# Performance work log

Hardware: AMD Instinct MI355X
Metric: run time of the kernel (lower is better)

The kernel has to match this reference:

```python
import jax, jax.numpy as jnp
import numpy as np

DIM = 128
HEADS = 4
POS_DIM = (DIM // 4) // 4  # DynamicPosBias: pos_dim = (dim//4)//4 = 8


def _layernorm(x, g, b, eps=1e-5):
    m = x.mean(-1, keepdims=True)
    v = x.var(-1, keepdims=True)
    return (x - m) / jnp.sqrt(v + eps) * g + b


def setup_inputs() -> dict:
    key = jax.random.key(0)
    ks = jax.random.split(key, 16)
    B_, N, C = 64, 512, DIM
    s = 0.02
    inp = {
        "x": jax.random.normal(ks[0], (B_, N, C), jnp.float32),
        "y": jax.random.normal(ks[1], (B_, N, C), jnp.float32),
        "H": 8, "W": 8, "D": 8,
        "qkv_w": jax.random.normal(ks[2], (3 * C, C), jnp.float32) * s,
        "qkv_b": jnp.zeros((3 * C,), jnp.float32),
        "proj_w": jax.random.normal(ks[3], (C, C), jnp.float32) * s,
        "proj_b": jnp.zeros((C,), jnp.float32),
        "pos_proj_w": jax.random.normal(ks[4], (POS_DIM, 3), jnp.float32) * s,
        "pos_proj_b": jnp.zeros((POS_DIM,), jnp.float32),
        "ln1_g": jnp.ones((POS_DIM,), jnp.float32),
        "ln1_b": jnp.zeros((POS_DIM,), jnp.float32),
        "p1_w": jax.random.normal(ks[5], (POS_DIM, POS_DIM), jnp.float32) * s,
        "p1_b": jnp.zeros((POS_DIM,), jnp.float32),
        "ln2_g": jnp.ones((POS_DIM,), jnp.float32),
        "ln2_b": jnp.zeros((POS_DIM,), jnp.float32),
        "p2_w": jax.random.normal(ks[6], (POS_DIM, POS_DIM), jnp.float32) * s,
        "p2_b": jnp.zeros((POS_DIM,), jnp.float32),
        "ln3_g": jnp.ones((POS_DIM,), jnp.float32),
        "ln3_b": jnp.zeros((POS_DIM,), jnp.float32),
        "p3_w": jax.random.normal(ks[7], (HEADS, POS_DIM), jnp.float32) * s,
        "p3_b": jnp.zeros((HEADS,), jnp.float32),
    }
    return inp


def _rel_pos_static(H, W, D):
    # biases table: all relative offsets, shape ((2H-1)(2W-1)(2D-1), 3)
    bh = np.arange(1 - H, H)
    bw = np.arange(1 - W, W)
    bd = np.arange(1 - D, D)
    biases = np.stack(np.meshgrid(bh, bw, bd, indexing="ij")).reshape(3, -1).T
    # relative position index, shape (N, N)
    coords = np.stack(np.meshgrid(np.arange(H), np.arange(W), np.arange(D), indexing="ij")).reshape(3, -1)
    rel = coords[:, :, None] - coords[:, None, :]  # (3, N, N)
    rel = rel.transpose(1, 2, 0).astype(np.int64)
    rel[:, :, 0] += H - 1
    rel[:, :, 1] += W - 1
    rel[:, :, 2] += D - 1
    rel[:, :, 0] *= (2 * W - 1) * (2 * D - 1)
    rel[:, :, 1] *= 2 * D - 1
    idx = rel.sum(-1)  # (N, N)
    return jnp.asarray(biases, jnp.float32), jnp.asarray(idx)


def reference(x, y, H, W, D, qkv_w, qkv_b, proj_w, proj_b,
              pos_proj_w, pos_proj_b, ln1_g, ln1_b, p1_w, p1_b,
              ln2_g, ln2_b, p2_w, p2_b, ln3_g, ln3_b, p3_w, p3_b):
    B_, N, C = x.shape
    h = p3_b.shape[0]
    hd = C // h
    scale = hd ** -0.5

    def qkv_fn(t):
        q3 = (t @ qkv_w.T + qkv_b).reshape(B_, N, 3, h, hd)
        q3 = q3.transpose(2, 0, 3, 1, 4)  # (3, B, h, N, hd)
        return q3[0], q3[1], q3[2]

    q, k, v = qkv_fn(x)
    # NOTE: original code uses self.qkv(y) (not qkv_y) -- reproduced faithfully
    q_y, k_y, v_y = qkv_fn(y)

    attn = jnp.einsum("bhnd,bhmd->bhnm", q * scale, k_y)  # (B, h, N, N)

    biases, idx = _rel_pos_static(H, W, D)
    # DynamicPosBias, residual=False: pos3(pos2(pos1(pos_proj(b))))
    pos = biases @ pos_proj_w.T + pos_proj_b
    pos = jax.nn.relu(_layernorm(pos, ln1_g, ln1_b)) @ p1_w.T + p1_b
    pos = jax.nn.relu(_layernorm(pos, ln2_g, ln2_b)) @ p2_w.T + p2_b
    pos = jax.nn.relu(_layernorm(pos, ln3_g, ln3_b)) @ p3_w.T + p3_b  # (table, h)
    rpb = pos[idx.reshape(-1)].reshape(N, N, h).transpose(2, 0, 1)  # (h, N, N)

    attn = jax.nn.softmax(attn + rpb[None], axis=-1)
    out = jnp.einsum("bhnm,bhmd->bhnd", attn, v_y)
    out = out.transpose(0, 2, 1, 3).reshape(B_, N, C)
    out = out @ proj_w.T + proj_b
    return out
```

## Files before the change

### kernel.cpp

```cpp
#include <hip/hip_runtime.h>
#include <hip/hip_bf16.h>

typedef __attribute__((ext_vector_type(4))) float f32x4;
typedef __attribute__((ext_vector_type(8))) short bf16x8;
typedef __attribute__((ext_vector_type(4))) short bf16x4;
typedef __attribute__((ext_vector_type(2))) unsigned int u32x2;

#define DEV static __device__ __forceinline__

constexpr float LOG2E  = 1.4426950408889634f;
constexpr float QSCALE = 0.17677669529663687f * LOG2E;

constexpr size_t OFF_Q   = 0;
constexpr size_t OFF_K   = (size_t)8  << 20;
constexpr size_t OFF_V   = (size_t)16 << 20;
constexpr size_t OFF_RPB = (size_t)24 << 20;
constexpr size_t OFF_AO  = (size_t)27 << 20;
constexpr size_t OFF_POS = (size_t)35 << 20;
constexpr size_t OFF_WQ  = (size_t)36 << 20;
constexpr size_t OFF_WP  = (size_t)37 << 20;

DEV short f2b(float f) {
  union { __bf16 h; short s; } u;
  u.h = (__bf16)f;
  return u.s;
}
DEV float b2f(unsigned int u) {
  union { unsigned int u; float f; } x; x.u = u; return x.f;
}
DEV unsigned int pkbf(float a, float b) {
  union { __bf16 h; unsigned short s; } ua, ub;
  ua.h = (__bf16)a; ub.h = (__bf16)b;
  return (unsigned int)ua.s | ((unsigned int)ub.s << 16);
}

DEV void ln_relu8(const float* v, const float* __restrict__ g,
                  const float* __restrict__ b, float* t) {
  float m = 0.f;
#pragma unroll
  for (int i = 0; i < 8; i++) m += v[i];
  m *= 0.125f;
  float var = 0.f;
#pragma unroll
  for (int i = 0; i < 8; i++) { float d = v[i] - m; var += d * d; }
  var *= 0.125f;
  float inv = 1.0f / sqrtf(var + 1e-5f);
#pragma unroll
  for (int i = 0; i < 8; i++) {
    float u = (v[i] - m) * inv * g[i] + b[i];
    t[i] = u > 0.f ? u : 0.f;
  }
}

DEV void mm8(const float* t, const float* __restrict__ w,
             const float* __restrict__ c, float* o) {
#pragma unroll
  for (int oo = 0; oo < 8; oo++) {
    float a = c[oo];
#pragma unroll
    for (int i = 0; i < 8; i++) a += t[i] * w[oo * 8 + i];
    o[oo] = a;
  }
}

__global__ void ca_setup(
    const float* __restrict__ qkv_w, const float* __restrict__ proj_w,
    short* __restrict__ wq, short* __restrict__ wp,
    const float* __restrict__ pw, const float* __restrict__ pb,
    const float* __restrict__ g1, const float* __restrict__ b1,
    const float* __restrict__ w1, const float* __restrict__ c1,
    const float* __restrict__ g2, const float* __restrict__ b2,
    const float* __restrict__ w2, const float* __restrict__ c2,
    const float* __restrict__ g3, const float* __restrict__ b3,
    const float* __restrict__ w3, const float* __restrict__ c3,
    float* __restrict__ pos_out) {
  const int blk = blockIdx.x;
  if (blk < 256) {
    int i = blk * 256 + threadIdx.x;
    if (i < 49152) {
      float f = qkv_w[i];
      if (i < 16384) f *= QSCALE;
      wq[i] = f2b(f);
    } else {
      wp[i - 49152] = f2b(proj_w[i - 49152]);
    }
    return;
  }
  int r = (blk - 256) * 256 + threadIdx.x;
  if (r >= 3375) return;
  float x0 = (float)(r / 225 - 7);
  float x1 = (float)((r / 15) % 15 - 7);
  float x2 = (float)(r % 15 - 7);
  float v[8], t[8], u[8];
#pragma unroll
  for (int o = 0; o < 8; o++)
    v[o] = x0 * pw[o * 3] + x1 * pw[o * 3 + 1] + x2 * pw[o * 3 + 2] + pb[o];
  ln_relu8(v, g1, b1, t);
  mm8(t, w1, c1, u);
  ln_relu8(u, g2, b2, t);
  mm8(t, w2, c2, v);
  ln_relu8(v, g3, b3, t);
#pragma unroll
  for (int hh = 0; hh < 4; hh++) {
    float a = c3[hh];
#pragma unroll
    for (int i = 0; i < 8; i++) a += t[i] * w3[hh * 8 + i];
    pos_out[r * 4 + hh] = a * LOG2E;
  }
}

__global__ __launch_bounds__(256) void ca_qkv_rpb(
    const float* __restrict__ x, const float* __restrict__ y,
    const short* __restrict__ wq, const float* __restrict__ qkv_b,
    short* __restrict__ gq, short* __restrict__ gk, short* __restrict__ gv,
    const float* __restrict__ posb, short* __restrict__ rpbf) {
  __shared__ short lds[16384];
  const int blk = blockIdx.x;
  const int tid = threadIdx.x;

  if (blk >= 1536) {
    int gid = (blk - 1536) * 256 + tid;
    int lane = gid & 63, jc = (gid >> 6) & 31, qg = (gid >> 11) & 31, hh = gid >> 16;
    int q = qg * 16 + (lane & 15);
    int j0 = jc * 16 + (lane >> 4) * 4;
    bf16x4 outv;
#pragma unroll
    for (int r = 0; r < 4; r++) {
      int j = j0 + r;
      int rh = (q >> 6) - (j >> 6) + 7;
      int rw = ((q >> 3) & 7) - ((j >> 3) & 7) + 7;
      int rd = (q & 7) - (j & 7) + 7;
      int idx = (rh * 15 + rw) * 15 + rd;
      outv[r] = f2b(posb[idx * 4 + hh]);
    }
    *(bf16x4*)(rpbf + (size_t)gid * 4) = outv;
    return;
  }

  const int z = blk >> 9;
  const int t0 = (blk & 511) * 64;
  const int b_ = t0 >> 9;
  const int n0 = t0 & 511;
  const float* __restrict__ in = (z == 0) ? x : y;
#pragma unroll
  for (int i = 0; i < 8; i++) {
    int flat = i * 1024 + tid * 4;
    f32x4 f = *(const f32x4*)(in + (size_t)t0 * 128 + flat);
    int row = flat >> 7, col = flat & 127;
    bf16x4 hv;
#pragma unroll
    for (int e = 0; e < 4; e++) hv[e] = f2b(f[e]);
    *(bf16x4*)(lds + row * 136 + col) = hv;
  }
  __syncthreads();
  const int w = tid >> 6, lane = tid & 63, lr = lane & 15, lg = lane >> 4;
  bf16x8 afrag[4];
  {
    const short* ap = lds + (w * 16 + lr) * 136 + lg * 8;
#pragma unroll
    for (int k4 = 0; k4 < 4; k4++) afrag[k4] = *(const bf16x8*)(ap + k4 * 32);
  }
  __syncthreads();

  if (z == 0) {
#pragma unroll
    for (int ct = 0; ct < 8; ct++) {
      const int col = ct * 16;
      float bias = qkv_b[col + lr] * QSCALE;
      f32x4 acc = {bias, bias, bias, bias};
      const short* bp = wq + (size_t)(col + lr) * 128 + lg * 8;
#pragma unroll
      for (int k4 = 0; k4 < 4; k4++) {
        bf16x8 bfr = *(const bf16x8*)(bp + k4 * 32);
        acc = __builtin_amdgcn_mfma_f32_16x16x32_bf16(afrag[k4], bfr, acc, 0, 0, 0);
      }
      const int d = (ct & 1) * 16 + lr;
      const int base = (w * 4 + (ct >> 1)) * 512 + 128 * (d >> 3) + (d & 7);
#pragma unroll
      for (int r = 0; r < 4; r++)
        lds[base + (lg * 4 + r) * 8] = f2b(acc[r]);
    }
  } else if (z == 1) {
#pragma unroll
    for (int ct = 0; ct < 8; ct++) {
      const int col = 128 + ct * 16;
      float bias = qkv_b[col + lr];
      f32x4 acc = {bias, bias, bias, bias};
      const short* bp = wq + (size_t)(col + lr) * 128 + lg * 8;
#pragma unroll
      for (int k4 = 0; k4 < 4; k4++) {
        bf16x8 bfr = *(const bf16x8*)(bp + k4 * 32);
        acc = __builtin_amdgcn_mfma_f32_16x16x32_bf16(afrag[k4], bfr, acc, 0, 0, 0);
      }
      const int d = (ct & 1) * 16 + lr;
      const int base = (w * 4 + (ct >> 1)) * 512 + 128 * (d >> 3) + (d & 7);
#pragma unroll
      for (int r = 0; r < 4; r++)
        lds[base + (lg * 4 + r) * 8] = f2b(acc[r]);
    }
  } else {
#pragma unroll
    for (int ct = 0; ct < 8; ct++) {
      const int col = 256 + ct * 16;
      float bias = qkv_b[col + lr];
      f32x4 acc = {bias, bias, bias, bias};
      const short* bp = wq + (size_t)(col + lr) * 128 + lg * 8;
#pragma unroll
      for (int k4 = 0; k4 < 4; k4++) {
        bf16x8 bfr = *(const bf16x8*)(bp + k4 * 32);
        acc = __builtin_amdgcn_mfma_f32_16x16x32_bf16(afrag[k4], bfr, acc, 0, 0, 0);
      }
      const int hv_ = ct >> 1;
      const int dh = ct & 1;
      const int base = 8192 + (((hv_ * 2 + (w >> 1)) * 2 + dh) * 512) + lane * 8 + (w & 1) * 4;
      *(unsigned int*)(lds + base)     = pkbf(acc[0], acc[1]);
      *(unsigned int*)(lds + base + 2) = pkbf(acc[2], acc[3]);
    }
  }
  __syncthreads();
  if (z == 0) {
#pragma unroll
    for (int kk = 0; kk < 4; kk++) {
      const int c = kk * 4 + w, hh = c & 3, tg = c >> 2;
      bf16x8 vd = *(const bf16x8*)(lds + c * 512 + lane * 8);
      *(bf16x8*)(gq + (((size_t)b_ * 4 + hh) * 32 + (n0 >> 4) + tg) * 512 + lane * 8) = vd;
    }
  } else if (z == 1) {
#pragma unroll
    for (int kk = 0; kk < 4; kk++) {
      const int c = kk * 4 + w, hh = c & 3, tg = c >> 2;
      bf16x8 vd = *(const bf16x8*)(lds + c * 512 + lane * 8);
      *(bf16x8*)(gk + (((size_t)b_ * 4 + hh) * 32 + (n0 >> 4) + tg) * 512 + lane * 8) = vd;
    }
  } else {
#pragma unroll
    for (int kk = 0; kk < 4; kk++) {
      const int c = kk * 4 + w, hh = c >> 2, ul = (c >> 1) & 1, dh = c & 1;
      bf16x8 vd = *(const bf16x8*)(lds + 8192 + c * 512 + lane * 8);
      *(bf16x8*)(gv + ((((size_t)b_ * 4 + hh) * 16 + (n0 >> 5) + ul) * 2 + dh) * 512 + lane * 8) = vd;
    }
  }
}

DEV void stage_kv8(const short* kg, const short* vg, short* buf, int T, int w, int lane) {
#pragma unroll
  for (int i = 0; i < 2; i++) {
    const int c = w * 2 + i;
    const short* src;
    short* dst;
    if (c < 8) {
      src = kg + ((size_t)(T * 8 + c)) * 512 + lane * 8;
      dst = buf + c * 512;
    } else {
      src = vg + ((size_t)(T * 8 + c - 8)) * 512 + lane * 8;
      dst = buf + 4096 + (c - 8) * 512;
    }
    __builtin_amdgcn_global_load_lds((const __attribute__((address_space(1))) void*)src,
                                     (__attribute__((address_space(3))) void*)dst, 16, 0, 0);
  }
}

__global__ __launch_bounds__(512, 8) void ca_attn(
    const short* __restrict__ qfrag, const short* __restrict__ kfrag,
    const short* __restrict__ vfrag, const short* __restrict__ rpbf,
    short* __restrict__ aob) {
  __shared__ short kv[2][8192];
  const int bid = blockIdx.x;
  const int qt2 = bid >> 8, rem = bid & 255;
  const int b_ = rem >> 2, hh = rem & 3;
  const int bh = b_ * 4 + hh;
  const int tid = threadIdx.x;
  const int w = tid >> 6, lane = tid & 63, lg = lane >> 4;
  const int qg = qt2 * 8 + w;
  const int q0 = qg * 16;

  const short* kg = kfrag + (size_t)bh * 16384;
  const short* vg = vfrag + (size_t)bh * 16384;
  const bf16x8 qf = *(const bf16x8*)(qfrag + ((size_t)bh * 32 + qg) * 512 + lane * 8);
  const short* bp = rpbf + ((size_t)(hh * 32 + qg) << 13) + lane * 4;

  union PU { bf16x8 v; unsigned int u[4]; };
  PU ones;
  ones.u[0] = 0x3F803F80u; ones.u[1] = 0x3F803F80u;
  ones.u[2] = 0x3F803F80u; ones.u[3] = 0x3F803F80u;

  stage_kv8(kg, vg, &kv[0][0], 0, w, lane);
  __syncthreads();

  f32x4 o0 = {0.f, 0.f, 0.f, 0.f}, o1 = {0.f, 0.f, 0.f, 0.f}, o2 = {0.f, 0.f, 0.f, 0.f};

  for (int T = 0; T < 4; T++) {
    const int cur = T & 1;
    if (T < 3) stage_kv8(kg, vg, &kv[cur ^ 1][0], T + 1, w, lane);
    const short* kt = &kv[cur][0];
    const short* vt = &kv[cur][4096];

    u32x2 bw[8];
#pragma unroll
    for (int t = 0; t < 8; t++) bw[t] = *(const u32x2*)(bp + (size_t)(T * 8 + t) * 256);

#pragma unroll
    for (int uu = 0; uu < 4; uu++) {
      PU p;
#pragma unroll
      for (int half = 0; half < 2; half++) {
        const int t = uu * 2 + half;
        bf16x8 kf = *(const bf16x8*)(kt + t * 512 + lane * 8);
        f32x4 cin;
        cin[0] = b2f(bw[t].x << 16);
        cin[1] = b2f(bw[t].x & 0xFFFF0000u);
        cin[2] = b2f(bw[t].y << 16);
        cin[3] = b2f(bw[t].y & 0xFFFF0000u);
        f32x4 s = __builtin_amdgcn_mfma_f32_16x16x32_bf16(kf, qf, cin, 0, 0, 0);
        p.u[half * 2 + 0] = pkbf(__builtin_exp2f(s[0]), __builtin_exp2f(s[1]));
        p.u[half * 2 + 1] = pkbf(__builtin_exp2f(s[2]), __builtin_exp2f(s[3]));
      }
      bf16x8 vf0 = *(const bf16x8*)(vt + (uu * 2 + 0) * 512 + lane * 8);
      bf16x8 vf1 = *(const bf16x8*)(vt + (uu * 2 + 1) * 512 + lane * 8);
      o0 = __builtin_amdgcn_mfma_f32_16x16x32_bf16(p.v, vf0, o0, 0, 0, 0);
      o1 = __builtin_amdgcn_mfma_f32_16x16x32_bf16(p.v, vf1, o1, 0, 0, 0);
      o2 = __builtin_amdgcn_mfma_f32_16x16x32_bf16(p.v, ones.v, o2, 0, 0, 0);
    }
    if (T < 3) __syncthreads();
  }

  short* pt = &kv[0][w * 1024];
  const int lr = lane & 15;
#pragma unroll
  for (int r = 0; r < 4; r++) {
    float iv = 1.0f / o2[r];
    pt[(lg * 4 + r) * 40 + lr] = f2b(o0[r] * iv);
    pt[(lg * 4 + r) * 40 + 16 + lr] = f2b(o1[r] * iv);
  }
  asm volatile("s_waitcnt lgkmcnt(0)" ::: "memory");
  __builtin_amdgcn_sched_barrier(0);
  {
    const int qq = lane >> 2, pp = lane & 3;
    bf16x8 od = *(const bf16x8*)(pt + qq * 40 + pp * 8);
    *(bf16x8*)(aob + ((size_t)bh * 512 + q0 + qq) * 32 + pp * 8) = od;
  }
}

__global__ __launch_bounds__(256) void ca_proj(
    const short* __restrict__ aob, const short* __restrict__ wp,
    const float* __restrict__ proj_b, float* __restrict__ out) {
  __shared__ float plds[8448];
  const int t0 = blockIdx.x * 64;
  const int b_ = t0 >> 9, n0 = t0 & 511;
  const int tid = threadIdx.x;
  const int w = tid >> 6, lane = tid & 63, lr = lane & 15, lg = lane >> 4;
  bf16x8 afrag[4];
#pragma unroll
  for (int k4 = 0; k4 < 4; k4++)
    afrag[k4] = *(const bf16x8*)(aob + (((size_t)b_ * 4 + k4) * 512 + n0 + w * 16 + lr) * 32 + lg * 8);
  float* pt = plds + w * 2112;
#pragma unroll
  for (int ct = 0; ct < 8; ct++) {
    float bias = proj_b[ct * 16 + lr];
    f32x4 acc = {bias, bias, bias, bias};
    const short* bp = wp + (size_t)(ct * 16 + lr) * 128 + lg * 8;
#pragma unroll
    for (int k4 = 0; k4 < 4; k4++) {
      bf16x8 bfr = *(const bf16x8*)(bp + k4 * 32);
      acc = __builtin_amdgcn_mfma_f32_16x16x32_bf16(afrag[k4], bfr, acc, 0, 0, 0);
    }
#pragma unroll
    for (int r = 0; r < 4; r++)
      pt[(lg * 4 + r) * 132 + ct * 16 + lr] = acc[r];
  }
  asm volatile("s_waitcnt lgkmcnt(0)" ::: "memory");
  __builtin_amdgcn_sched_barrier(0);
#pragma unroll
  for (int i = 0; i < 8; i++) {
    int f = i * 256 + lane * 4;
    int row = f >> 7, col = f & 127;
    f32x4 v = *(const f32x4*)(pt + row * 132 + col);
    *(f32x4*)(out + (size_t)(t0 + w * 16) * 128 + f) = v;
  }
}

extern "C" void kernel_launch(void* const* d_in, const int* in_sizes, int n_in,
                              void* d_out, int out_size, void* d_ws, size_t ws_size,
                              hipStream_t stream) {
  const float* x      = (const float*)d_in[0];
  const float* y      = (const float*)d_in[1];
  const float* qkv_w  = (const float*)d_in[5];
  const float* qkv_b  = (const float*)d_in[6];
  const float* proj_w = (const float*)d_in[7];
  const float* proj_b = (const float*)d_in[8];
  const float* pos_w  = (const float*)d_in[9];
  const float* pos_b  = (const float*)d_in[10];
  const float* ln1g = (const float*)d_in[11];
  const float* ln1b = (const float*)d_in[12];
  const float* p1w  = (const float*)d_in[13];
  const float* p1b  = (const float*)d_in[14];
  const float* ln2g = (const float*)d_in[15];
  const float* ln2b = (const float*)d_in[16];
  const float* p2w  = (const float*)d_in[17];
  const float* p2b  = (const float*)d_in[18];
  const float* ln3g = (const float*)d_in[19];
  const float* ln3b = (const float*)d_in[20];
  const float* p3w  = (const float*)d_in[21];
  const float* p3b  = (const float*)d_in[22];
  float* out = (float*)d_out;

  char* ws = (char*)d_ws;
  short* gq    = (short*)(ws + OFF_Q);
  short* gk    = (short*)(ws + OFF_K);
  short* gv    = (short*)(ws + OFF_V);
  short* rpbf  = (short*)(ws + OFF_RPB);
  short* aob   = (short*)(ws + OFF_AO);
  float* posb  = (float*)(ws + OFF_POS);
  short* wq    = (short*)(ws + OFF_WQ);
  short* wp    = (short*)(ws + OFF_WP);

  ca_setup<<<270, 256, 0, stream>>>(qkv_w, proj_w, wq, wp,
                                    pos_w, pos_b, ln1g, ln1b, p1w, p1b,
                                    ln2g, ln2b, p2w, p2b, ln3g, ln3b, p3w, p3b, posb);
  ca_qkv_rpb<<<2560, 256, 0, stream>>>(x, y, wq, qkv_b, gq, gk, gv, posb, rpbf);
  ca_attn<<<1024, 512, 0, stream>>>(gq, gk, gv, rpbf, aob);
  ca_proj<<<512, 256, 0, stream>>>(aob, wp, proj_b, out);
}
```

Before: 78.29 us.

## Fuse attention and output projection into one kernel looping over heads

Merges the attention kernel and the output projection kernel. Each block now handles all four heads for a 128-query tile and keeps the per-head outputs in registers as projection A-fragments, so the attention output never goes to global memory and one launch is removed. In exchange the grid drops from 1024 to 256 blocks and each block runs four times longer with a serial head loop, which lowers parallelism and occupancy on a GPU with many CUs.

```diff
diff --git a/kernel.cpp b/kernel.cpp
--- a/kernel.cpp
+++ b/kernel.cpp
@@ -15,7 +15,6 @@
 constexpr size_t OFF_K   = (size_t)8  << 20;
 constexpr size_t OFF_V   = (size_t)16 << 20;
 constexpr size_t OFF_RPB = (size_t)24 << 20;
-constexpr size_t OFF_AO  = (size_t)27 << 20;
 constexpr size_t OFF_POS = (size_t)35 << 20;
 constexpr size_t OFF_WQ  = (size_t)36 << 20;
 constexpr size_t OFF_WP  = (size_t)37 << 20;
@@ -242,7 +241,7 @@
   }
 }
 
-DEV void stage_kv8(const short* kg, const short* vg, short* buf, int T, int w, int lane) {
+DEV void stage_s(const short* kg, const short* vg, short* buf, int T, int w, int lane) {
 #pragma unroll
   for (int i = 0; i < 2; i++) {
     const int c = w * 2 + i;
@@ -260,122 +259,119 @@
   }
 }
 
-__global__ __launch_bounds__(512, 8) void ca_attn(
+__global__ __launch_bounds__(512, 2) void ca_attn_proj(
     const short* __restrict__ qfrag, const short* __restrict__ kfrag,
     const short* __restrict__ vfrag, const short* __restrict__ rpbf,
-    short* __restrict__ aob) {
+    const short* __restrict__ wp, const float* __restrict__ proj_b,
+    float* __restrict__ out) {
   __shared__ short kv[2][8192];
+  __shared__ short ptile[8][640];
   const int bid = blockIdx.x;
-  const int qt2 = bid >> 8, rem = bid & 255;
-  const int b_ = rem >> 2, hh = rem & 3;
-  const int bh = b_ * 4 + hh;
+  const int qt2 = bid >> 6, b_ = bid & 63;
   const int tid = threadIdx.x;
-  const int w = tid >> 6, lane = tid & 63, lg = lane >> 4;
+  const int w = tid >> 6, lane = tid & 63, lg = lane >> 4, lr = lane & 15;
   const int qg = qt2 * 8 + w;
   const int q0 = qg * 16;
-
-  const short* kg = kfrag + (size_t)bh * 16384;
-  const short* vg = vfrag + (size_t)bh * 16384;
-  const bf16x8 qf = *(const bf16x8*)(qfrag + ((size_t)bh * 32 + qg) * 512 + lane * 8);
-  const short* bp = rpbf + ((size_t)(hh * 32 + qg) << 13) + lane * 4;
 
   union PU { bf16x8 v; unsigned int u[4]; };
   PU ones;
   ones.u[0] = 0x3F803F80u; ones.u[1] = 0x3F803F80u;
   ones.u[2] = 0x3F803F80u; ones.u[3] = 0x3F803F80u;
 
-  stage_kv8(kg, vg, &kv[0][0], 0, w, lane);
+  stage_s(kfrag + (size_t)(b_ * 4) * 16384, vfrag + (size_t)(b_ * 4) * 16384,
+          &kv[0][0], 0, w, lane);
   __syncthreads();
 
-  f32x4 o0 = {0.f, 0.f, 0.f, 0.f}, o1 = {0.f, 0.f, 0.f, 0.f}, o2 = {0.f, 0.f, 0.f, 0.f};
-
-  for (int T = 0; T < 4; T++) {
-    const int cur = T & 1;
-    if (T < 3) stage_kv8(kg, vg, &kv[cur ^ 1][0], T + 1, w, lane);
-    const short* kt = &kv[cur][0];
-    const short* vt = &kv[cur][4096];
-
-    u32x2 bw[8];
-#pragma unroll
-    for (int t = 0; t < 8; t++) bw[t] = *(const u32x2*)(bp + (size_t)(T * 8 + t) * 256);
-
-#pragma unroll
-    for (int uu = 0; uu < 4; uu++) {
-      PU p;
-#pragma unroll
-      for (int half = 0; half < 2; half++) {
-        const int t = uu * 2 + half;
-        bf16x8 kf = *(const bf16x8*)(kt + t * 512 + lane * 8);
-        f32x4 cin;
-        cin[0] = b2f(bw[t].x << 16);
-        cin[1] = b2f(bw[t].x & 0xFFFF0000u);
-        cin[2] = b2f(bw[t].y << 16);
-        cin[3] = b2f(bw[t].y & 0xFFFF0000u);
-        f32x4 s = __builtin_amdgcn_mfma_f32_16x16x32_bf16(kf, qf, cin, 0, 0, 0);
-        p.u[half * 2 + 0] = pkbf(__builtin_exp2f(s[0]), __builtin_exp2f(s[1]));
-        p.u[half * 2 + 1] = pkbf(__builtin_exp2f(s[2]), __builtin_exp2f(s[3]));
-      }
-      bf16x8 vf0 = *(const bf16x8*)(vt + (uu * 2 + 0) * 512 + lane * 8);
-      bf16x8 vf1 = *(const bf16x8*)(vt + (uu * 2 + 1) * 512 + lane * 8);
-      o0 = __builtin_amdgcn_mfma_f32_16x16x32_bf16(p.v, vf0, o0, 0, 0, 0);
-      o1 = __builtin_amdgcn_mfma_f32_16x16x32_bf16(p.v, vf1, o1, 0, 0, 0);
-      o2 = __builtin_amdgcn_mfma_f32_16x16x32_bf16(p.v, ones.v, o2, 0, 0, 0);
-    }
-    if (T < 3) __syncthreads();
-  }
-
-  short* pt = &kv[0][w * 1024];
-  const int lr = lane & 15;
-#pragma unroll
-  for (int r = 0; r < 4; r++) {
-    float iv = 1.0f / o2[r];
-    pt[(lg * 4 + r) * 40 + lr] = f2b(o0[r] * iv);
-    pt[(lg * 4 + r) * 40 + 16 + lr] = f2b(o1[r] * iv);
-  }
-  asm volatile("s_waitcnt lgkmcnt(0)" ::: "memory");
-  __builtin_amdgcn_sched_barrier(0);
-  {
-    const int qq = lane >> 2, pp = lane & 3;
-    bf16x8 od = *(const bf16x8*)(pt + qq * 40 + pp * 8);
-    *(bf16x8*)(aob + ((size_t)bh * 512 + q0 + qq) * 32 + pp * 8) = od;
-  }
-}
-
-__global__ __launch_bounds__(256) void ca_proj(
-    const short* __restrict__ aob, const short* __restrict__ wp,
-    const float* __restrict__ proj_b, float* __restrict__ out) {
-  __shared__ float plds[8448];
-  const int t0 = blockIdx.x * 64;
-  const int b_ = t0 >> 9, n0 = t0 & 511;
-  const int tid = threadIdx.x;
-  const int w = tid >> 6, lane = tid & 63, lr = lane & 15, lg = lane >> 4;
-  bf16x8 afrag[4];
-#pragma unroll
-  for (int k4 = 0; k4 < 4; k4++)
-    afrag[k4] = *(const bf16x8*)(aob + (((size_t)b_ * 4 + k4) * 512 + n0 + w * 16 + lr) * 32 + lg * 8);
-  float* pt = plds + w * 2112;
-#pragma unroll
-  for (int ct = 0; ct < 8; ct++) {
-    float bias = proj_b[ct * 16 + lr];
-    f32x4 acc = {bias, bias, bias, bias};
-    const short* bp = wp + (size_t)(ct * 16 + lr) * 128 + lg * 8;
-#pragma unroll
-    for (int k4 = 0; k4 < 4; k4++) {
-      bf16x8 bfr = *(const bf16x8*)(bp + k4 * 32);
-      acc = __builtin_amdgcn_mfma_f32_16x16x32_bf16(afrag[k4], bfr, acc, 0, 0, 0);
-    }
-#pragma unroll
-    for (int r = 0; r < 4; r++)
-      pt[(lg * 4 + r) * 132 + ct * 16 + lr] = acc[r];
-  }
-  asm volatile("s_waitcnt lgkmcnt(0)" ::: "memory");
-  __builtin_amdgcn_sched_barrier(0);
-#pragma unroll
-  for (int i = 0; i < 8; i++) {
-    int f = i * 256 + lane * 4;
-    int row = f >> 7, col = f & 127;
-    f32x4 v = *(const f32x4*)(pt + row * 132 + col);
-    *(f32x4*)(out + (size_t)(t0 + w * 16) * 128 + f) = v;
+  bf16x8 af[4];
+  short* pt = &ptile[w][0];
+
+#pragma unroll
+  for (int h = 0; h < 4; h++) {
+    const int bh = b_ * 4 + h;
+    const bf16x8 qf = *(const bf16x8*)(qfrag + ((size_t)bh * 32 + qg) * 512 + lane * 8);
+    const short* bp = rpbf + ((size_t)(h * 32 + qg) << 13) + lane * 4;
+
+    f32x4 o0 = {0.f, 0.f, 0.f, 0.f}, o1 = {0.f, 0.f, 0.f, 0.f}, o2 = {0.f, 0.f, 0.f, 0.f};
+
+#pragma unroll
+    for (int T = 0; T < 4; T++) {
+      const int s = h * 4 + T;
+      if (s < 15) {
+        const int sn = s + 1, hn = sn >> 2, Tn = sn & 3;
+        stage_s(kfrag + (size_t)(b_ * 4 + hn) * 16384, vfrag + (size_t)(b_ * 4 + hn) * 16384,
+                &kv[sn & 1][0], Tn, w, lane);
+      }
+      const short* kt = &kv[s & 1][0];
+      const short* vt = &kv[s & 1][4096];
+
+      u32x2 bw[8];
+#pragma unroll
+      for (int t = 0; t < 8; t++) bw[t] = *(const u32x2*)(bp + (size_t)(T * 8 + t) * 256);
+
+#pragma unroll
+      for (int uu = 0; uu < 4; uu++) {
+        PU p;
+#pragma unroll
+        for (int half = 0; half < 2; half++) {
+          const int t = uu * 2 + half;
+          bf16x8 kf = *(const bf16x8*)(kt + t * 512 + lane * 8);
+          f32x4 cin;
+          cin[0] = b2f(bw[t].x << 16);
+          cin[1] = b2f(bw[t].x & 0xFFFF0000u);
+          cin[2] = b2f(bw[t].y << 16);
+          cin[3] = b2f(bw[t].y & 0xFFFF0000u);
+          f32x4 s2 = __builtin_amdgcn_mfma_f32_16x16x32_bf16(kf, qf, cin, 0, 0, 0);
+          p.u[half * 2 + 0] = pkbf(__builtin_exp2f(s2[0]), __builtin_exp2f(s2[1]));
+          p.u[half * 2 + 1] = pkbf(__builtin_exp2f(s2[2]), __builtin_exp2f(s2[3]));
+        }
+        bf16x8 vf0 = *(const bf16x8*)(vt + (uu * 2 + 0) * 512 + lane * 8);
+        bf16x8 vf1 = *(const bf16x8*)(vt + (uu * 2 + 1) * 512 + lane * 8);
+        o0 = __builtin_amdgcn_mfma_f32_16x16x32_bf16(p.v, vf0, o0, 0, 0, 0);
+        o1 = __builtin_amdgcn_mfma_f32_16x16x32_bf16(p.v, vf1, o1, 0, 0, 0);
+        o2 = __builtin_amdgcn_mfma_f32_16x16x32_bf16(p.v, ones.v, o2, 0, 0, 0);
+      }
+      if (s < 15) __syncthreads();
+    }
+
+#pragma unroll
+    for (int r = 0; r < 4; r++) {
+      float iv = 1.0f / o2[r];
+      pt[(lg * 4 + r) * 40 + lr] = f2b(o0[r] * iv);
+      pt[(lg * 4 + r) * 40 + 16 + lr] = f2b(o1[r] * iv);
+    }
+    asm volatile("s_waitcnt lgkmcnt(0)" ::: "memory");
+    __builtin_amdgcn_sched_barrier(0);
+    af[h] = *(const bf16x8*)(pt + lr * 40 + lg * 8);
+  }
+
+  __syncthreads();
+  float* fpt = (float*)(&kv[0][0]) + w * 1024;
+#pragma unroll
+  for (int p = 0; p < 2; p++) {
+#pragma unroll
+    for (int c4 = 0; c4 < 4; c4++) {
+      const int ct = p * 4 + c4;
+      float bias = proj_b[ct * 16 + lr];
+      f32x4 acc = {bias, bias, bias, bias};
+      const short* bpw = wp + (size_t)(ct * 16 + lr) * 128 + lg * 8;
+#pragma unroll
+      for (int k4 = 0; k4 < 4; k4++) {
+        bf16x8 bfr = *(const bf16x8*)(bpw + k4 * 32);
+        acc = __builtin_amdgcn_mfma_f32_16x16x32_bf16(af[k4], bfr, acc, 0, 0, 0);
+      }
+#pragma unroll
+      for (int r = 0; r < 4; r++)
+        fpt[(lg * 4 + r) * 64 + c4 * 16 + lr] = acc[r];
+    }
+    asm volatile("s_waitcnt lgkmcnt(0)" ::: "memory");
+    __builtin_amdgcn_sched_barrier(0);
+#pragma unroll
+    for (int i = 0; i < 4; i++) {
+      f32x4 v = *(const f32x4*)(fpt + i * 256 + lane * 4);
+      const int row = i * 4 + (lane >> 4);
+      const int col = (lane & 15) * 4;
+      *(f32x4*)(out + (size_t)(b_ * 512 + qt2 * 128 + w * 16 + row) * 128 + p * 64 + col) = v;
+    }
   }
 }
 
@@ -409,7 +405,6 @@
   short* gk    = (short*)(ws + OFF_K);
   short* gv    = (short*)(ws + OFF_V);
   short* rpbf  = (short*)(ws + OFF_RPB);
-  short* aob   = (short*)(ws + OFF_AO);
   float* posb  = (float*)(ws + OFF_POS);
   short* wq    = (short*)(ws + OFF_WQ);
   short* wp    = (short*)(ws + OFF_WP);
@@ -418,6 +413,5 @@
                                     pos_w, pos_b, ln1g, ln1b, p1w, p1b,
                                     ln2g, ln2b, p2w, p2b, ln3g, ln3b, p3w, p3b, posb);
   ca_qkv_rpb<<<2560, 256, 0, stream>>>(x, y, wq, qkv_b, gq, gk, gv, posb, rpbf);
-  ca_attn<<<1024, 512, 0, stream>>>(gq, gk, gv, rpbf, aob);
-  ca_proj<<<512, 256, 0, stream>>>(aob, wp, proj_b, out);
-}
+  ca_attn_proj<<<256, 512, 0, stream>>>(gq, gk, gv, rpbf, wp, proj_b, out);
+}
```

Result: slower. 86.08 us (+9.9%).
